# Performance work log

Measured on AMD Instinct MI355X. Metric: run time of the kernel, lower is better.

The kernel has to match this reference:

```python
import jax, jax.numpy as jnp
import numpy as np

B_, DIM, NPTS = 16, 128, 16384
J, K, L = 16, 128, 128   # kernel_mode, GkNN_mode_out, GkNN_mode_in
R, M1, M2 = 8, 64, 64    # low-rank A/B dims and mask modes


def setup_inputs() -> dict:
    key = jax.random.key(0)
    ks = jax.random.split(key, 9)
    scale = 1.0 / (L * K)
    return {
        "x": jax.random.normal(ks[0], (B_, DIM, NPTS), jnp.float32),
        "bases": jax.random.normal(ks[1], (NPTS, K), jnp.float32),
        "wbases": jax.random.normal(ks[2], (NPTS, L), jnp.float32),
        "product": jax.random.normal(ks[3], (K, L), jnp.float32),
        "D_out": jax.random.normal(ks[4], (J, K), jnp.float32),
        "D_in": jax.random.normal(ks[5], (J, L), jnp.float32),
        "A": jax.random.normal(ks[6], (J, R, M1), jnp.float32),
        "B": jax.random.normal(ks[7], (J, R, M2), jnp.float32),
        "weights": scale * jax.random.normal(ks[8], (DIM, DIM, J), jnp.float32),
    }


def reference(x, bases, wbases, product, D_out, D_in, A, B, weights):
    # project onto weighted bases: (b, c, npts) @ (npts, L) -> (b, c, L)
    x_hat = jnp.einsum('bcx,xl->bcl', x, wbases)
    # H tensor: (J, K, L) broadcast product + low-rank correction
    H = D_out[:, :, None] * D_in[:, None, :] * product[None, :, :]
    Q = jnp.einsum('jrm,jrn->jmn', A, B)  # bmm(A^T, B): (J, M1, M2)
    H = H.at[:, :Q.shape[1], :Q.shape[2]].add(Q)
    # mode mixing: (J,K,L) x (b,i,L) -> (b,i,J,K), then weights (i,o,J)
    x_hat1 = jnp.einsum('jkl,bil->bijk', H, x_hat)
    y = jnp.einsum('ioj,bijk->bok', weights, x_hat1)
    # back to physical space: (b, o, K) x (npts, K) -> (b, o, npts)
    return jnp.einsum('bok,xk->box', y, bases)
```

## Files before the change

### kernel.cpp

```cpp
#include <hip/hip_runtime.h>

#define B_    16
#define DIM   128
#define NPTS  16384
#define J_    16
#define K_    128
#define L_    128
#define R_    8
#define M1_   64

typedef float  f32x4 __attribute__((ext_vector_type(4)));
typedef short  s16x8 __attribute__((ext_vector_type(8)));
typedef unsigned short u16;
typedef u16 u16x8 __attribute__((ext_vector_type(8)));
typedef u16 u16x4 __attribute__((ext_vector_type(4)));

__device__ __forceinline__ u16 f2bf(float f) {
    unsigned u = __float_as_uint(f);
    u += 0x7FFFu + ((u >> 16) & 1u);
    return (u16)(u >> 16);
}
#define MFMA16(a,b,c) __builtin_amdgcn_mfma_f32_16x16x32_bf16((a),(b),(c),0,0,0)

#define OFF_PARTA 0u
#define OFF_WBT   8388608u
#define OFF_BASB  12582912u
#define OFF_HKL   16777216u
#define OFF_W2T   17301504u
#define OFF_XHB   17825792u
#define OFF_YB    18350080u
#define OFF_YP    18874368u

__global__ __launch_bounds__(256) void k_prep(
    const float* __restrict__ product, const float* __restrict__ Do,
    const float* __restrict__ Di, const float* __restrict__ A,
    const float* __restrict__ Bm, const float* __restrict__ W,
    const float* __restrict__ wb, const float* __restrict__ bases,
    u16* __restrict__ Hkl, u16* __restrict__ W2T,
    u16* __restrict__ wbT, u16* __restrict__ basesb)
{
    __shared__ u16 sT[128][136];
    const int bid = blockIdx.x, t = threadIdx.x;
    if (bid < 1024) {
        int idx = (bid << 8) | t;
        int j = idx >> 14, k = (idx >> 7) & 127, l = idx & 127;
        float v = Do[j*K_ + k] * Di[j*L_ + l] * product[k*L_ + l];
        if (k < M1_ && l < M1_) {
            float q = 0.f;
            #pragma unroll
            for (int r = 0; r < R_; ++r)
                q += A[(j*R_ + r)*M1_ + k] * Bm[(j*R_ + r)*M1_ + l];
            v += q;
        }
        Hkl[idx] = f2bf(v);
    } else if (bid < 2048) {
        int idx = ((bid - 1024) << 8) | t;
        int o = idx >> 11, ji = idx & 2047, j = ji >> 7, i = ji & 127;
        W2T[idx] = f2bf(W[(i*DIM + o)*J_ + j]);
    } else if (bid < 2176) {
        const int p0 = (bid - 2048) * 128;
        #pragma unroll
        for (int it = 0; it < 16; ++it) {
            int idx = it*256 + t, row = idx >> 5, c4 = (idx & 31) * 4;
            float4 v = *(const float4*)(wb + (size_t)(p0+row)*L_ + c4);
            sT[c4+0][row] = f2bf(v.x); sT[c4+1][row] = f2bf(v.y);
            sT[c4+2][row] = f2bf(v.z); sT[c4+3][row] = f2bf(v.w);
        }
        __syncthreads();
        #pragma unroll
        for (int it = 0; it < 8; ++it) {
            int idx = it*256 + t, l = idx >> 4, pc = (idx & 15) * 8;
            *(u16x8*)(wbT + (size_t)l*NPTS + p0 + pc) = *(const u16x8*)&sT[l][pc];
        }
    } else {
        int i = (((bid - 2176) << 8) | t) * 4;
        float4 v = *(const float4*)(bases + i);
        u16x4 o4 = { f2bf(v.x), f2bf(v.y), f2bf(v.z), f2bf(v.w) };
        *(u16x4*)(basesb + i) = o4;
    }
}

__global__ __launch_bounds__(512) void k_stageA(
    const float* __restrict__ x, const u16* __restrict__ wbT,
    float* __restrict__ part)
{
    __shared__ u16 sA[64][136];
    __shared__ u16 sB[128][136];
    const int t = threadIdx.x, lane = t & 63, wave = t >> 6;
    const int quad = lane >> 4, l16 = lane & 15;
    const int wr = wave >> 2, wc = wave & 3;
    const int m0 = blockIdx.x * 64;
    const size_t pbase = (size_t)blockIdx.y * 2048;

    f32x4 acc[2][2] = {};
    const int ac4 = (t & 31) * 4, arr = t >> 5;
    const int bc8 = (t & 15) * 8, brr = t >> 4;

    for (int pc = 0; pc < 2048; pc += 128) {
        #pragma unroll
        for (int i = 0; i < 4; ++i) {
            int row = arr + 16*i;
            float4 v = *(const float4*)(x + (size_t)(m0+row)*NPTS + pbase + pc + ac4);
            u16x4 h = { f2bf(v.x), f2bf(v.y), f2bf(v.z), f2bf(v.w) };
            *(u16x4*)&sA[row][ac4] = h;
        }
        #pragma unroll
        for (int i = 0; i < 4; ++i) {
            int row = brr + 32*i;
            *(u16x8*)&sB[row][bc8] =
                *(const u16x8*)(wbT + (size_t)row*NPTS + pbase + pc + bc8);
        }
        __syncthreads();
        #pragma unroll
        for (int ks = 0; ks < 4; ++ks) {
            int kb = ks*32 + quad*8;
            s16x8 a0 = *(const s16x8*)&sA[wr*32      + l16][kb];
            s16x8 a1 = *(const s16x8*)&sA[wr*32 + 16 + l16][kb];
            s16x8 b0 = *(const s16x8*)&sB[wc*32      + l16][kb];
            s16x8 b1 = *(const s16x8*)&sB[wc*32 + 16 + l16][kb];
            acc[0][0] = MFMA16(a0, b0, acc[0][0]);
            acc[0][1] = MFMA16(a0, b1, acc[0][1]);
            acc[1][0] = MFMA16(a1, b0, acc[1][0]);
            acc[1][1] = MFMA16(a1, b1, acc[1][1]);
        }
        __syncthreads();
    }
    float* po = part + (size_t)blockIdx.y * (2048*128);
    #pragma unroll
    for (int mt = 0; mt < 2; ++mt)
      #pragma unroll
      for (int r = 0; r < 4; ++r) {
        int row = m0 + wr*32 + mt*16 + quad*4 + r;
        #pragma unroll
        for (int nt = 0; nt < 2; ++nt) {
            int col = wc*32 + nt*16 + l16;
            po[(size_t)row*128 + col] = acc[mt][nt][r];
        }
      }
}

__global__ __launch_bounds__(256) void k_reduceA(
    const float* __restrict__ part, u16* __restrict__ xhatb)
{
    int i = blockIdx.x * 1024 + threadIdx.x;
    #pragma unroll
    for (int e = 0; e < 4; ++e, i += 256) {
        float s = 0.f;
        #pragma unroll
        for (int p = 0; p < 8; ++p) s += part[p*262144 + i];
        xhatb[i] = f2bf(s);
    }
}

__global__ __launch_bounds__(256) void k_mix1(
    const u16* __restrict__ Hkl, const u16* __restrict__ xhatb,
    u16* __restrict__ Tt)
{
    __shared__ u16 sA[128][136];
    __shared__ u16 sB[128][136];
    const int t = threadIdx.x, lane = t & 63, wave = t >> 6;
    const int quad = lane >> 4, l16 = lane & 15;
    const int wr = wave >> 1, wc = wave & 1;
    const int b = blockIdx.x, j = blockIdx.y;
    const u16* ha = Hkl + j*16384;
    const u16* xb = xhatb + b*16384;

    const int c8 = (t & 15)*8, rr = t >> 4;
    #pragma unroll
    for (int i = 0; i < 8; ++i) {
        int row = rr + 16*i;
        *(u16x8*)&sA[row][c8] = *(const u16x8*)(ha + row*128 + c8);
        *(u16x8*)&sB[row][c8] = *(const u16x8*)(xb + row*128 + c8);
    }
    __syncthreads();

    f32x4 acc[4][4] = {};
    #pragma unroll
    for (int ks = 0; ks < 4; ++ks) {
        int kb = ks*32 + quad*8;
        s16x8 a[4], bf[4];
        #pragma unroll
        for (int mt = 0; mt < 4; ++mt) a[mt]  = *(const s16x8*)&sA[wr*64 + mt*16 + l16][kb];
        #pragma unroll
        for (int nt = 0; nt < 4; ++nt) bf[nt] = *(const s16x8*)&sB[wc*64 + nt*16 + l16][kb];
        #pragma unroll
        for (int mt = 0; mt < 4; ++mt)
            #pragma unroll
            for (int nt = 0; nt < 4; ++nt)
                acc[mt][nt] = MFMA16(a[mt], bf[nt], acc[mt][nt]);
    }
    u16* to = Tt + (size_t)b*262144 + (j << 7);
    #pragma unroll
    for (int mt = 0; mt < 4; ++mt)
      #pragma unroll
      for (int r = 0; r < 4; ++r) {
        int k = wr*64 + mt*16 + quad*4 + r;
        #pragma unroll
        for (int nt = 0; nt < 4; ++nt) {
            int i = wc*64 + nt*16 + l16;
            to[(size_t)k*2048 + i] = f2bf(acc[mt][nt][r]);
        }
      }
}

__global__ __launch_bounds__(256) void k_mix2(
    const u16* __restrict__ W2T, const u16* __restrict__ Tt,
    float* __restrict__ ypart)
{
    __shared__ u16 sA[128][136];
    __shared__ u16 sB[128][136];
    const int t = threadIdx.x, lane = t & 63, wave = t >> 6;
    const int quad = lane >> 4, l16 = lane & 15;
    const int wr = wave >> 1, wc = wave & 1;
    const int b = blockIdx.x, c = blockIdx.y;
    const int ji0 = c * 128;
    const u16* tb = Tt + (size_t)b*262144;

    const int c8 = (t & 15)*8, rr = t >> 4;
    #pragma unroll
    for (int i = 0; i < 8; ++i) {
        int row = rr + 16*i;
        *(u16x8*)&sA[row][c8] = *(const u16x8*)(W2T + (size_t)row*2048 + ji0 + c8);
        *(u16x8*)&sB[row][c8] = *(const u16x8*)(tb  + (size_t)row*2048 + ji0 + c8);
    }
    __syncthreads();

    f32x4 acc[4][4] = {};
    #pragma unroll
    for (int ks = 0; ks < 4; ++ks) {
        int kb = ks*32 + quad*8;
        s16x8 a[4], bf[4];
        #pragma unroll
        for (int mt = 0; mt < 4; ++mt) a[mt]  = *(const s16x8*)&sA[wr*64 + mt*16 + l16][kb];
        #pragma unroll
        for (int nt = 0; nt < 4; ++nt) bf[nt] = *(const s16x8*)&sB[wc*64 + nt*16 + l16][kb];
        #pragma unroll
        for (int mt = 0; mt < 4; ++mt)
            #pragma unroll
            for (int nt = 0; nt < 4; ++nt)
                acc[mt][nt] = MFMA16(a[mt], bf[nt], acc[mt][nt]);
    }
    float* yo = ypart + ((size_t)(c*16 + b) << 14);
    #pragma unroll
    for (int mt = 0; mt < 4; ++mt)
      #pragma unroll
      for (int r = 0; r < 4; ++r) {
        int o = wr*64 + mt*16 + quad*4 + r;
        #pragma unroll
        for (int nt = 0; nt < 4; ++nt) {
            int k = wc*64 + nt*16 + l16;
            yo[(size_t)o*128 + k] = acc[mt][nt][r];
        }
      }
}

__global__ __launch_bounds__(256) void k_reduceY(
    const float* __restrict__ part, u16* __restrict__ yb)
{
    int i = blockIdx.x * 1024 + threadIdx.x;
    #pragma unroll
    for (int e = 0; e < 4; ++e, i += 256) {
        float s = 0.f;
        #pragma unroll
        for (int p = 0; p < 16; ++p) s += part[p*262144 + i];
        yb[i] = f2bf(s);
    }
}

__global__ __launch_bounds__(256) void k_stageE(
    const u16* __restrict__ yb, const u16* __restrict__ basesb,
    float* __restrict__ out)
{
    __shared__ u16 sA[128][136];
    __shared__ u16 sB[128][136];
    const int t = threadIdx.x, lane = t & 63, wave = t >> 6;
    const int quad = lane >> 4, l16 = lane & 15;
    const int wr = wave >> 1, wc = wave & 1;
    const int bo0 = blockIdx.x * 128, p0 = blockIdx.y * 128;

    const int c8 = (t & 15)*8, rr = t >> 4;
    #pragma unroll
    for (int i = 0; i < 8; ++i) {
        int row = rr + 16*i;
        *(u16x8*)&sA[row][c8] = *(const u16x8*)(yb     + (size_t)(bo0+row)*128 + c8);
        *(u16x8*)&sB[row][c8] = *(const u16x8*)(basesb + (size_t)(p0 +row)*128 + c8);
    }
    __syncthreads();

    f32x4 acc[4][4] = {};
    #pragma unroll
    for (int ks = 0; ks < 4; ++ks) {
        int kb = ks*32 + quad*8;
        s16x8 a[4], bf[4];
        #pragma unroll
        for (int mt = 0; mt < 4; ++mt) a[mt]  = *(const s16x8*)&sA[wr*64 + mt*16 + l16][kb];
        #pragma unroll
        for (int nt = 0; nt < 4; ++nt) bf[nt] = *(const s16x8*)&sB[wc*64 + nt*16 + l16][kb];
        #pragma unroll
        for (int mt = 0; mt < 4; ++mt)
            #pragma unroll
            for (int nt = 0; nt < 4; ++nt)
                acc[mt][nt] = MFMA16(a[mt], bf[nt], acc[mt][nt]);
    }
    #pragma unroll
    for (int mt = 0; mt < 4; ++mt)
      #pragma unroll
      for (int r = 0; r < 4; ++r) {
        size_t row = bo0 + wr*64 + mt*16 + quad*4 + r;
        #pragma unroll
        for (int nt = 0; nt < 4; ++nt) {
            int p = p0 + wc*64 + nt*16 + l16;
            out[row*NPTS + p] = acc[mt][nt][r];
        }
      }
}

extern "C" void kernel_launch(void* const* d_in, const int* in_sizes, int n_in,
                              void* d_out, int out_size, void* d_ws, size_t ws_size,
                              hipStream_t stream) {
    (void)in_sizes; (void)n_in; (void)out_size; (void)ws_size;
    const float* x       = (const float*)d_in[0];
    const float* bases   = (const float*)d_in[1];
    const float* wbases  = (const float*)d_in[2];
    const float* product = (const float*)d_in[3];
    const float* Do      = (const float*)d_in[4];
    const float* Di      = (const float*)d_in[5];
    const float* A       = (const float*)d_in[6];
    const float* Bm      = (const float*)d_in[7];
    const float* W       = (const float*)d_in[8];

    char* ws = (char*)d_ws;
    float* partA  = (float*)(ws + OFF_PARTA);
    u16*   Tt     = (u16*)  (ws + OFF_PARTA);
    u16*   wbT    = (u16*)  (ws + OFF_WBT);
    u16*   basesb = (u16*)  (ws + OFF_BASB);
    u16*   Hkl    = (u16*)  (ws + OFF_HKL);
    u16*   W2T    = (u16*)  (ws + OFF_W2T);
    u16*   xhatb  = (u16*)  (ws + OFF_XHB);
    u16*   yb     = (u16*)  (ws + OFF_YB);
    float* ypart  = (float*)(ws + OFF_YP);

    k_prep   <<<4224, 256, 0, stream>>>(product, Do, Di, A, Bm, W, wbases, bases,
                                        Hkl, W2T, wbT, basesb);
    k_stageA <<<dim3(32, 8), 512, 0, stream>>>(x, wbT, partA);
    k_reduceA<<<256, 256, 0, stream>>>(partA, xhatb);
    k_mix1   <<<dim3(16, 16), 256, 0, stream>>>(Hkl, xhatb, Tt);
    k_mix2   <<<dim3(16, 16), 256, 0, stream>>>(W2T, Tt, ypart);
    k_reduceY<<<256, 256, 0, stream>>>(ypart, yb);
    k_stageE <<<dim3(16, 128), 256, 0, stream>>>(yb, basesb, (float*)d_out);
}
```

Measured before the change: 317.7 us.

## Double-buffer stageA loads, vectorize reductions, split mix kernels across more blocks

Stage A now double-buffers its LDS tiles: it prefetches the next x and wbT chunk into registers while running MFMAs on the current one, and uses one barrier per iteration instead of two. The partial-sum reductions use float4 loads with one element group per thread. The mix1 and mix2 kernels split the M dimension across a third grid axis, giving 512 blocks instead of 256 for better CU occupancy. The price is more register pressure in stage A and the B tiles being reloaded by twice as many blocks in the mix kernels.

```diff
diff --git a/kernel.cpp b/kernel.cpp
--- a/kernel.cpp
+++ b/kernel.cpp
@@ -84,8 +84,8 @@
     const float* __restrict__ x, const u16* __restrict__ wbT,
     float* __restrict__ part)
 {
-    __shared__ u16 sA[64][136];
-    __shared__ u16 sB[128][136];
+    __shared__ u16 sA[2][64][136];
+    __shared__ u16 sB[2][128][136];
     const int t = threadIdx.x, lane = t & 63, wave = t >> 6;
     const int quad = lane >> 4, l16 = lane & 15;
     const int wr = wave >> 2, wc = wave & 3;
@@ -96,35 +96,59 @@
     const int ac4 = (t & 31) * 4, arr = t >> 5;
     const int bc8 = (t & 15) * 8, brr = t >> 4;
 
-    for (int pc = 0; pc < 2048; pc += 128) {
-        #pragma unroll
-        for (int i = 0; i < 4; ++i) {
-            int row = arr + 16*i;
-            float4 v = *(const float4*)(x + (size_t)(m0+row)*NPTS + pbase + pc + ac4);
-            u16x4 h = { f2bf(v.x), f2bf(v.y), f2bf(v.z), f2bf(v.w) };
-            *(u16x4*)&sA[row][ac4] = h;
-        }
-        #pragma unroll
-        for (int i = 0; i < 4; ++i) {
-            int row = brr + 32*i;
-            *(u16x8*)&sB[row][bc8] =
-                *(const u16x8*)(wbT + (size_t)row*NPTS + pbase + pc + bc8);
-        }
+    #pragma unroll
+    for (int i = 0; i < 4; ++i) {
+        int row = arr + 16*i;
+        float4 v = *(const float4*)(x + (size_t)(m0+row)*NPTS + pbase + ac4);
+        u16x4 h = { f2bf(v.x), f2bf(v.y), f2bf(v.z), f2bf(v.w) };
+        *(u16x4*)&sA[0][row][ac4] = h;
+    }
+    #pragma unroll
+    for (int i = 0; i < 4; ++i) {
+        int row = brr + 32*i;
+        *(u16x8*)&sB[0][row][bc8] =
+            *(const u16x8*)(wbT + (size_t)row*NPTS + pbase + bc8);
+    }
+
+    int cur = 0;
+    for (int c = 0; c < 16; ++c) {
         __syncthreads();
+        float4 vx[4]; u16x8 vb[4];
+        if (c < 15) {
+            const size_t pb = pbase + (size_t)(c+1)*128;
+            #pragma unroll
+            for (int i = 0; i < 4; ++i)
+                vx[i] = *(const float4*)(x + (size_t)(m0+arr+16*i)*NPTS + pb + ac4);
+            #pragma unroll
+            for (int i = 0; i < 4; ++i)
+                vb[i] = *(const u16x8*)(wbT + (size_t)(brr+32*i)*NPTS + pb + bc8);
+        }
         #pragma unroll
         for (int ks = 0; ks < 4; ++ks) {
             int kb = ks*32 + quad*8;
-            s16x8 a0 = *(const s16x8*)&sA[wr*32      + l16][kb];
-            s16x8 a1 = *(const s16x8*)&sA[wr*32 + 16 + l16][kb];
-            s16x8 b0 = *(const s16x8*)&sB[wc*32      + l16][kb];
-            s16x8 b1 = *(const s16x8*)&sB[wc*32 + 16 + l16][kb];
+            s16x8 a0 = *(const s16x8*)&sA[cur][wr*32      + l16][kb];
+            s16x8 a1 = *(const s16x8*)&sA[cur][wr*32 + 16 + l16][kb];
+            s16x8 b0 = *(const s16x8*)&sB[cur][wc*32      + l16][kb];
+            s16x8 b1 = *(const s16x8*)&sB[cur][wc*32 + 16 + l16][kb];
             acc[0][0] = MFMA16(a0, b0, acc[0][0]);
             acc[0][1] = MFMA16(a0, b1, acc[0][1]);
             acc[1][0] = MFMA16(a1, b0, acc[1][0]);
             acc[1][1] = MFMA16(a1, b1, acc[1][1]);
         }
-        __syncthreads();
-    }
+        if (c < 15) {
+            int nxt = cur ^ 1;
+            #pragma unroll
+            for (int i = 0; i < 4; ++i) {
+                u16x4 h = { f2bf(vx[i].x), f2bf(vx[i].y), f2bf(vx[i].z), f2bf(vx[i].w) };
+                *(u16x4*)&sA[nxt][arr+16*i][ac4] = h;
+            }
+            #pragma unroll
+            for (int i = 0; i < 4; ++i)
+                *(u16x8*)&sB[nxt][brr+32*i][bc8] = vb[i];
+        }
+        cur ^= 1;
+    }
+
     float* po = part + (size_t)blockIdx.y * (2048*128);
     #pragma unroll
     for (int mt = 0; mt < 2; ++mt)
@@ -142,59 +166,65 @@
 __global__ __launch_bounds__(256) void k_reduceA(
     const float* __restrict__ part, u16* __restrict__ xhatb)
 {
-    int i = blockIdx.x * 1024 + threadIdx.x;
-    #pragma unroll
-    for (int e = 0; e < 4; ++e, i += 256) {
-        float s = 0.f;
-        #pragma unroll
-        for (int p = 0; p < 8; ++p) s += part[p*262144 + i];
-        xhatb[i] = f2bf(s);
-    }
+    const float4* p4 = (const float4*)part;
+    int i = blockIdx.x * 256 + threadIdx.x;
+    float4 s = {0.f, 0.f, 0.f, 0.f};
+    #pragma unroll
+    for (int p = 0; p < 8; ++p) {
+        float4 v = p4[(size_t)p*65536 + i];
+        s.x += v.x; s.y += v.y; s.z += v.z; s.w += v.w;
+    }
+    u16x4 o4 = { f2bf(s.x), f2bf(s.y), f2bf(s.z), f2bf(s.w) };
+    *(u16x4*)(xhatb + (size_t)i*4) = o4;
 }
 
 __global__ __launch_bounds__(256) void k_mix1(
     const u16* __restrict__ Hkl, const u16* __restrict__ xhatb,
     u16* __restrict__ Tt)
 {
-    __shared__ u16 sA[128][136];
+    __shared__ u16 sA[64][136];
     __shared__ u16 sB[128][136];
     const int t = threadIdx.x, lane = t & 63, wave = t >> 6;
     const int quad = lane >> 4, l16 = lane & 15;
     const int wr = wave >> 1, wc = wave & 1;
-    const int b = blockIdx.x, j = blockIdx.y;
-    const u16* ha = Hkl + j*16384;
+    const int b = blockIdx.x, j = blockIdx.y, kh = blockIdx.z;
+    const u16* ha = Hkl + j*16384 + kh*64*128;
     const u16* xb = xhatb + b*16384;
 
     const int c8 = (t & 15)*8, rr = t >> 4;
     #pragma unroll
+    for (int i = 0; i < 4; ++i) {
+        int row = rr + 16*i;
+        *(u16x8*)&sA[row][c8] = *(const u16x8*)(ha + row*128 + c8);
+    }
+    #pragma unroll
     for (int i = 0; i < 8; ++i) {
         int row = rr + 16*i;
-        *(u16x8*)&sA[row][c8] = *(const u16x8*)(ha + row*128 + c8);
         *(u16x8*)&sB[row][c8] = *(const u16x8*)(xb + row*128 + c8);
     }
     __syncthreads();
 
-    f32x4 acc[4][4] = {};
+    f32x4 acc[2][4] = {};
     #pragma unroll
     for (int ks = 0; ks < 4; ++ks) {
         int kb = ks*32 + quad*8;
-        s16x8 a[4], bf[4];
-        #pragma unroll
-        for (int mt = 0; mt < 4; ++mt) a[mt]  = *(const s16x8*)&sA[wr*64 + mt*16 + l16][kb];
+        s16x8 a[2], bf[4];
+        #pragma unroll
+        for (int mt = 0; mt < 2; ++mt) a[mt]  = *(const s16x8*)&sA[wr*32 + mt*16 + l16][kb];
         #pragma unroll
         for (int nt = 0; nt < 4; ++nt) bf[nt] = *(const s16x8*)&sB[wc*64 + nt*16 + l16][kb];
         #pragma unroll
-        for (int mt = 0; mt < 4; ++mt)
+        for (int mt = 0; mt < 2; ++mt)
             #pragma unroll
             for (int nt = 0; nt < 4; ++nt)
                 acc[mt][nt] = MFMA16(a[mt], bf[nt], acc[mt][nt]);
     }
     u16* to = Tt + (size_t)b*262144 + (j << 7);
     #pragma unroll
-    for (int mt = 0; mt < 4; ++mt)
+    for (int mt = 0; mt < 2; ++mt)
       #pragma unroll
       for (int r = 0; r < 4; ++r) {
-        int k = wr*64 + mt*16 + quad*4 + r;
+        int k = kh*64 + wr*32 + mt*16 + quad*4 + r;
         #pragma unroll
         for (int nt = 0; nt < 4; ++nt) {
             int i = wc*64 + nt*16 + l16;
@@ -207,45 +237,49 @@
     const u16* __restrict__ W2T, const u16* __restrict__ Tt,
     float* __restrict__ ypart)
 {
-    __shared__ u16 sA[128][136];
+    __shared__ u16 sA[64][136];
     __shared__ u16 sB[128][136];
     const int t = threadIdx.x, lane = t & 63, wave = t >> 6;
     const int quad = lane >> 4, l16 = lane & 15;
     const int wr = wave >> 1, wc = wave & 1;
-    const int b = blockIdx.x, c = blockIdx.y;
+    const int b = blockIdx.x, c = blockIdx.y, oh = blockIdx.z;
     const int ji0 = c * 128;
     const u16* tb = Tt + (size_t)b*262144;
 
     const int c8 = (t & 15)*8, rr = t >> 4;
     #pragma unroll
+    for (int i = 0; i < 4; ++i) {
+        int row = rr + 16*i;
+        *(u16x8*)&sA[row][c8] = *(const u16x8*)(W2T + (size_t)(oh*64+row)*2048 + ji0 + c8);
+    }
+    #pragma unroll
     for (int i = 0; i < 8; ++i) {
         int row = rr + 16*i;
-        *(u16x8*)&sA[row][c8] = *(const u16x8*)(W2T + (size_t)row*2048 + ji0 + c8);
-        *(u16x8*)&sB[row][c8] = *(const u16x8*)(tb  + (size_t)row*2048 + ji0 + c8);
+        *(u16x8*)&sB[row][c8] = *(const u16x8*)(tb + (size_t)row*2048 + ji0 + c8);
     }
     __syncthreads();
 
-    f32x4 acc[4][4] = {};
+    f32x4 acc[2][4] = {};
     #pragma unroll
     for (int ks = 0; ks < 4; ++ks) {
         int kb = ks*32 + quad*8;
-        s16x8 a[4], bf[4];
-        #pragma unroll
-        for (int mt = 0; mt < 4; ++mt) a[mt]  = *(const s16x8*)&sA[wr*64 + mt*16 + l16][kb];
+        s16x8 a[2], bf[4];
+        #pragma unroll
+        for (int mt = 0; mt < 2; ++mt) a[mt]  = *(const s16x8*)&sA[wr*32 + mt*16 + l16][kb];
         #pragma unroll
         for (int nt = 0; nt < 4; ++nt) bf[nt] = *(const s16x8*)&sB[wc*64 + nt*16 + l16][kb];
         #pragma unroll
-        for (int mt = 0; mt < 4; ++mt)
+        for (int mt = 0; mt < 2; ++mt)
             #pragma unroll
             for (int nt = 0; nt < 4; ++nt)
                 acc[mt][nt] = MFMA16(a[mt], bf[nt], acc[mt][nt]);
     }
     float* yo = ypart + ((size_t)(c*16 + b) << 14);
     #pragma unroll
-    for (int mt = 0; mt < 4; ++mt)
+    for (int mt = 0; mt < 2; ++mt)
       #pragma unroll
       for (int r = 0; r < 4; ++r) {
-        int o = wr*64 + mt*16 + quad*4 + r;
+        int o = oh*64 + wr*32 + mt*16 + quad*4 + r;
         #pragma unroll
         for (int nt = 0; nt < 4; ++nt) {
             int k = wc*64 + nt*16 + l16;
@@ -257,14 +291,16 @@
 __global__ __launch_bounds__(256) void k_reduceY(
     const float* __restrict__ part, u16* __restrict__ yb)
 {
-    int i = blockIdx.x * 1024 + threadIdx.x;
-    #pragma unroll
-    for (int e = 0; e < 4; ++e, i += 256) {
-        float s = 0.f;
-        #pragma unroll
-        for (int p = 0; p < 16; ++p) s += part[p*262144 + i];
-        yb[i] = f2bf(s);
-    }
+    const float4* p4 = (const float4*)part;
+    int i = blockIdx.x * 256 + threadIdx.x;
+    float4 s = {0.f, 0.f, 0.f, 0.f};
+    #pragma unroll
+    for (int p = 0; p < 16; ++p) {
+        float4 v = p4[(size_t)p*65536 + i];
+        s.x += v.x; s.y += v.y; s.z += v.z; s.w += v.w;
+    }
+    u16x4 o4 = { f2bf(s.x), f2bf(s.y), f2bf(s.z), f2bf(s.w) };
+    *(u16x4*)(yb + (size_t)i*4) = o4;
 }
 
 __global__ __launch_bounds__(256) void k_stageE(
@@ -344,8 +380,8 @@
                                         Hkl, W2T, wbT, basesb);
     k_stageA <<<dim3(32, 8), 512, 0, stream>>>(x, wbT, partA);
     k_reduceA<<<256, 256, 0, stream>>>(partA, xhatb);
-    k_mix1   <<<dim3(16, 16), 256, 0, stream>>>(Hkl, xhatb, Tt);
-    k_mix2   <<<dim3(16, 16), 256, 0, stream>>>(W2T, Tt, ypart);
+    k_mix1   <<<dim3(16, 16, 2), 256, 0, stream>>>(Hkl, xhatb, Tt);
+    k_mix2   <<<dim3(16, 16, 2), 256, 0, stream>>>(W2T, Tt, ypart);
     k_reduceY<<<256, 256, 0, stream>>>(ypart, yb);
     k_stageE <<<dim3(16, 128), 256, 0, stream>>>(yb, basesb, (float*)d_out);
 }
```

Result: no change. 318.4 us (+0.2%).
